# Performance work log

Measured on AMD Instinct MI355X. Metric: run time of the kernel, lower is better.

The kernel has to match this reference:

```python
import jax, jax.numpy as jnp
import numpy as np

STRIDE = (1, 1)
PAD = (1, 1)
DIL = (1, 1)
KH, KW = 3, 3
DEFORM_GROUPS = 2


def setup_inputs() -> dict:
    key = jax.random.key(0)
    ks = jax.random.split(key, 5)
    B, C, H, W = 4, 128, 64, 64
    Cout = 128
    K = KH * KW
    n = C * KH * KW
    stdv = 1.0 / np.sqrt(n)
    x = jax.random.normal(ks[0], (B, C, H, W), dtype=jnp.float32)
    offset = jax.random.normal(ks[1], (B, DEFORM_GROUPS * 2 * K, H, W), dtype=jnp.float32)
    mask = jax.random.uniform(ks[2], (B, DEFORM_GROUPS * K, H, W), dtype=jnp.float32)
    weight = jax.random.uniform(ks[3], (Cout, C, KH, KW), minval=-stdv, maxval=stdv, dtype=jnp.float32)
    bias = jnp.zeros((Cout,), dtype=jnp.float32)
    return {"x": x, "offset": offset, "mask": mask, "weight": weight, "bias": bias}


def _mdcn_forward(x, offset, mask, weight, bias):
    B, C, H, W = x.shape
    Cout, Cin_g, kh, kw = weight.shape
    K = kh * kw
    dg = offset.shape[1] // (2 * K)
    Cg = C // dg
    sh, sw = STRIDE
    ph, pw = PAD
    dh, dw = DIL
    Ho = (H + 2 * ph - (dh * (kh - 1) + 1)) // sh + 1
    Wo = (W + 2 * pw - (dw * (kw - 1) + 1)) // sw + 1

    # offsets: (B, dg, K, 2, Ho, Wo) with (dy, dx) pairs; mask: (B, dg, K, Ho, Wo)
    off = offset.reshape(B, dg, K, 2, Ho, Wo)
    m = mask.reshape(B, dg, K, Ho, Wo)

    ky, kx = jnp.meshgrid(jnp.arange(kh), jnp.arange(kw), indexing="ij")
    ky = ky.reshape(K).astype(x.dtype)  # kernel tap row offsets
    kx = kx.reshape(K).astype(x.dtype)
    oy = (jnp.arange(Ho) * sh - ph).astype(x.dtype)
    ox = (jnp.arange(Wo) * sw - pw).astype(x.dtype)

    # sampling positions (B, dg, K, Ho, Wo)
    py = off[:, :, :, 0] + oy[None, None, None, :, None] + (ky * dh)[None, None, :, None, None]
    px = off[:, :, :, 1] + ox[None, None, None, None, :] + (kx * dw)[None, None, :, None, None]

    y0 = jnp.floor(py)
    x0 = jnp.floor(px)
    ly = py - y0
    lx = px - x0
    y0i = y0.astype(jnp.int32)
    x0i = x0.astype(jnp.int32)

    xg = x.reshape(B, dg, Cg, H * W)

    def gather(yi, xi):
        valid = (yi >= 0) & (yi < H) & (xi >= 0) & (xi < W)
        idx = jnp.clip(yi, 0, H - 1) * W + jnp.clip(xi, 0, W - 1)  # (B,dg,K,Ho,Wo)
        g = jax.vmap(jax.vmap(lambda xf, ix: xf[:, ix]))(xg, idx.reshape(B, dg, K * Ho * Wo))
        g = g.reshape(B, dg, Cg, K, Ho, Wo)
        return g * valid[:, :, None].astype(x.dtype)

    w00 = ((1 - ly) * (1 - lx))[:, :, None]
    w01 = ((1 - ly) * lx)[:, :, None]
    w10 = (ly * (1 - lx))[:, :, None]
    w11 = (ly * lx)[:, :, None]

    val = (w00 * gather(y0i, x0i)
           + w01 * gather(y0i, x0i + 1)
           + w10 * gather(y0i + 1, x0i)
           + w11 * gather(y0i + 1, x0i + 1))

    # modulation and im2col-GEMM (groups=1): col (B, C*K, Ho*Wo)
    col = (val * m[:, :, None]).reshape(B, C * K, Ho * Wo)
    wk = weight.reshape(Cout, C * K)
    out = jnp.einsum("ok,bkp->bop", wk, col).reshape(B, Cout, Ho, Wo)
    return out + bias[None, :, None, None]


def reference(x, offset, mask, weight, bias):
    return _mdcn_forward(x, offset, mask, weight, bias)
```

## Files before the change

### kernel.cpp

```cpp
#include <hip/hip_runtime.h>
#include <hip/hip_fp16.h>

#define B_    4
#define C_    128
#define H_    64
#define W_    64
#define CO_   128
#define K_    9
#define DG_   2
#define HW_   4096
#define CK_   1152
#define NKT_  36
#define NPAIR_ 576
#define PSTR_ 68
#define PLSZ_ 4352

typedef __attribute__((ext_vector_type(8))) short  short8;
typedef __attribute__((ext_vector_type(4))) float  floatx4;
typedef float f2v __attribute__((ext_vector_type(2), aligned(4)));

__device__ __align__(16) unsigned short g_wA[NKT_ * 8 * 64 * 8];
__device__ __align__(16) unsigned int   g_colu[(size_t)B_ * 128 * NPAIR_ * 32];
__device__ __align__(16) int4           g_desc[B_ * DG_ * K_ * HW_];

__device__ __forceinline__ unsigned short f32_to_bf16(float f) {
    unsigned int u = __float_as_uint(f);
    u += 0x7FFFu + ((u >> 16) & 1u);
    return (unsigned short)(u >> 16);
}
__device__ __forceinline__ unsigned int pack_bf16x2(float a, float b) {
    return (unsigned int)f32_to_bf16(a) | ((unsigned int)f32_to_bf16(b) << 16);
}

__global__ __launch_bounds__(256) void prep_kernel(
    const float* __restrict__ w,
    const float* __restrict__ offset,
    const float* __restrict__ mask)
{
    const int bid = blockIdx.x;
    if (bid < 576) {
        const int lin  = bid * 256 + threadIdx.x;
        const int j    = lin & 7;
        const int lane = (lin >> 3) & 63;
        const int mtkt = lin >> 9;
        const int mt   = mtkt & 7;
        const int kt   = mtkt >> 3;
        const int co   = mt * 16 + (lane & 15);
        const int k    = kt * 32 + (lane >> 4) * 8 + j;
        g_wA[lin] = f32_to_bf16(w[co * CK_ + k]);
    } else {
        const int lin = (bid - 576) * 256 + threadIdx.x;
        const int pix = lin & (HW_ - 1);
        const int bgk = lin >> 12;
        const int k   = bgk % 9;
        const int bg  = bgk / 9;
        const int ho = pix >> 6;
        const int wo = pix & 63;
        const int ky = k / 3;
        const int kx = k - 3 * ky;

        const float py = offset[(size_t)(bg * 18 + 2 * k)     * HW_ + pix] + (float)(ho - 1 + ky);
        const float px = offset[(size_t)(bg * 18 + 2 * k + 1) * HW_ + pix] + (float)(wo - 1 + kx);
        const float m  = mask  [(size_t)(bg * 9 + k)          * HW_ + pix];

        const float y0f = floorf(py);
        const float x0f = floorf(px);
        const float ly = py - y0f;
        const float lx = px - x0f;
        const int y0 = (int)y0f;
        const int x0 = (int)x0f;

        const bool yin = (y0 >= 0) & (y0 <= H_ - 2);
        const float er0 = yin ? (1.0f - ly) : ((y0 == -1)     ? ly          : 0.0f);
        const float er1 = yin ? ly          : ((y0 == H_ - 1) ? (1.0f - ly) : 0.0f);
        const bool xin = (x0 >= 0) & (x0 <= W_ - 2);
        const float ec0 = xin ? (1.0f - lx) : ((x0 == -1)     ? lx          : 0.0f);
        const float ec1 = xin ? lx          : ((x0 == W_ - 1) ? (1.0f - lx) : 0.0f);
        const int yc = min(max(y0, 0), H_ - 2);
        const int xc = min(max(x0, 0), W_ - 2);

        const __half2 wlo = __floats2half2_rn(m * er0 * ec0, m * er0 * ec1);
        const __half2 whi = __floats2half2_rn(m * er1 * ec0, m * er1 * ec1);
        int4 d;
        d.x = yc * PSTR_ + xc;
        d.y = __builtin_bit_cast(int, wlo);
        d.z = __builtin_bit_cast(int, whi);
        d.w = 0;
        g_desc[lin] = d;
    }
}

__global__ __launch_bounds__(1024, 4) void col_kernel(const float* __restrict__ x)
{
    const int bid = blockIdx.x;
    const int b   = bid >> 6;
    const int cp  = bid & 63;
    const int c0  = cp * 2;
    const int g   = c0 >> 6;
    const int t   = threadIdx.x;

    __shared__ __align__(16) float s_x[2 * PLSZ_];

    {
        const int ci = t >> 9;
        const int q  = t & 511;
        const float* __restrict__ src = x + (size_t)(b * C_ + c0 + ci) * HW_ + q * 8;
        const float4 v0 = *(const float4*)src;
        const float4 v1 = *(const float4*)(src + 4);
        float* dst = s_x + ci * PLSZ_ + (q >> 3) * PSTR_ + (q & 7) * 8;
        *(float4*)dst = v0;
        *(float4*)(dst + 4) = v1;
    }
    __syncthreads();

    const int4* __restrict__ descb = g_desc + (size_t)((b * DG_ + g) * 9) * HW_;

#pragma unroll
    for (int ps = 0; ps < 4; ++ps) {
        const int pix = ps * 1024 + t;
        const int pt  = pix >> 5;
        const int pl  = pix & 31;
        int4 d[9];
#pragma unroll
        for (int k = 0; k < 9; ++k) d[k] = descb[(size_t)k * HW_ + pix];

        float v[18];
#pragma unroll
        for (int k = 0; k < 9; ++k) {
            const float2 wl = __half22float2(__builtin_bit_cast(__half2, d[k].y));
            const float2 wh = __half22float2(__builtin_bit_cast(__half2, d[k].z));
#pragma unroll
            for (int ci = 0; ci < 2; ++ci) {
                const float* p = s_x + ci * PLSZ_ + d[k].x;
                const f2v lo = *(const f2v*)p;
                const f2v hi = *(const f2v*)(p + PSTR_);
                v[ci * 9 + k] = wl.x * lo.x + wl.y * lo.y + wh.x * hi.x + wh.y * hi.y;
            }
        }
        unsigned int* __restrict__ outb =
            g_colu + ((size_t)(b * 128 + pt) * NPAIR_ + cp * 9) * 32 + pl;
#pragma unroll
        for (int j = 0; j < 9; ++j)
            outb[j * 32] = pack_bf16x2(v[2 * j], v[2 * j + 1]);
    }
}

__global__ __launch_bounds__(512) void gemm_kernel(
    const float* __restrict__ bias, float* __restrict__ out)
{
    const int bid  = blockIdx.x;
    const int b    = bid >> 7;
    const int pt   = bid & 127;
    const int t    = threadIdx.x;
    const int w    = t >> 6;
    const int cw   = w >> 1;
    const int nt   = w & 1;
    const int lane = t & 63;
    const int l15  = lane & 15;
    const int quad = lane >> 4;

    const unsigned short* __restrict__ ap = g_wA + ((size_t)(cw * 2) * 64 + lane) * 8;
    const unsigned int* __restrict__ bp =
        g_colu + ((size_t)(b * 128 + pt) * NPAIR_ + quad * 4) * 32 + nt * 16 + l15;

    floatx4 acc0 = {0.f, 0.f, 0.f, 0.f};
    floatx4 acc1 = {0.f, 0.f, 0.f, 0.f};

    short8 a0c = *(const short8*)ap;
    short8 a1c = *(const short8*)(ap + 512);
    uint4 u0;
    u0.x = bp[0]; u0.y = bp[32]; u0.z = bp[64]; u0.w = bp[96];
    short8 b_c = __builtin_bit_cast(short8, u0);

#pragma unroll 4
    for (int kt = 0; kt < NKT_; ++kt) {
        short8 a0n = a0c, a1n = a1c, b_n = b_c;
        if (kt < NKT_ - 1) {
            const unsigned short* an = ap + (size_t)(kt + 1) * 4096;
            a0n = *(const short8*)an;
            a1n = *(const short8*)(an + 512);
            const unsigned int* bq = bp + (size_t)(kt + 1) * 512;
            uint4 u;
            u.x = bq[0]; u.y = bq[32]; u.z = bq[64]; u.w = bq[96];
            b_n = __builtin_bit_cast(short8, u);
        }
        acc0 = __builtin_amdgcn_mfma_f32_16x16x32_bf16(a0c, b_c, acc0, 0, 0, 0);
        acc1 = __builtin_amdgcn_mfma_f32_16x16x32_bf16(a1c, b_c, acc1, 0, 0, 0);
        a0c = a0n; a1c = a1n; b_c = b_n;
    }

#pragma unroll
    for (int mtl = 0; mtl < 2; ++mtl) {
        const floatx4 a = mtl ? acc1 : acc0;
        const int cob = cw * 32 + mtl * 16 + quad * 4;
#pragma unroll
        for (int r = 0; r < 4; ++r) {
            const int co = cob + r;
            out[((size_t)(b * CO_ + co) << 12) + pt * 32 + nt * 16 + l15] = a[r] + bias[co];
        }
    }
}

extern "C" void kernel_launch(void* const* d_in, const int* in_sizes, int n_in,
                              void* d_out, int out_size, void* d_ws, size_t ws_size,
                              hipStream_t stream) {
    const float* x      = (const float*)d_in[0];
    const float* offset = (const float*)d_in[1];
    const float* mask   = (const float*)d_in[2];
    const float* weight = (const float*)d_in[3];
    const float* bias   = (const float*)d_in[4];
    float* out = (float*)d_out;

    hipLaunchKernelGGL(prep_kernel, dim3(576 + 1152), dim3(256), 0, stream, weight, offset, mask);
    hipLaunchKernelGGL(col_kernel, dim3(B_ * 64), dim3(1024), 0, stream, x);
    hipLaunchKernelGGL(gemm_kernel, dim3(B_ * 128), dim3(512), 0, stream, bias, out);
}
```

Measured before the change: 102.6 us.

## Stage four fp16 channels per shared texel and reorder GEMM K dimension tap-major

The col kernel now loads four channels into shared memory as packed fp16 vectors, so one bilinear descriptor fetch serves four channels and each corner read is a single 8-byte LDS load. The block split changes to 4-channel by quarter-image tiles with one pixel per thread. The reduction dimension is reordered tap-major, with weights permuted to match. The GEMM uses 64-pixel tiles with 16 waves per block. Storing x in fp16 adds some precision loss, and there are fewer, larger GEMM blocks.

```diff
diff --git a/kernel.cpp b/kernel.cpp
--- a/kernel.cpp
+++ b/kernel.cpp
@@ -12,15 +12,14 @@
 #define CK_   1152
 #define NKT_  36
 #define NPAIR_ 576
-#define PSTR_ 68
-#define PLSZ_ 4352
-
-typedef __attribute__((ext_vector_type(8))) short  short8;
-typedef __attribute__((ext_vector_type(4))) float  floatx4;
-typedef float f2v __attribute__((ext_vector_type(2), aligned(4)));
+#define XSTR_ 68
+
+typedef __attribute__((ext_vector_type(8))) short    short8;
+typedef __attribute__((ext_vector_type(4))) float    floatx4;
+typedef __attribute__((ext_vector_type(4))) _Float16 h4v;
 
 __device__ __align__(16) unsigned short g_wA[NKT_ * 8 * 64 * 8];
-__device__ __align__(16) unsigned int   g_colu[(size_t)B_ * 128 * NPAIR_ * 32];
+__device__ __align__(16) unsigned int   g_colu[(size_t)B_ * 64 * NPAIR_ * 64];
 __device__ __align__(16) int4           g_desc[B_ * DG_ * K_ * HW_];
 
 __device__ __forceinline__ unsigned short f32_to_bf16(float f) {
@@ -46,8 +45,10 @@
         const int mt   = mtkt & 7;
         const int kt   = mtkt >> 3;
         const int co   = mt * 16 + (lane & 15);
-        const int k    = kt * 32 + (lane >> 4) * 8 + j;
-        g_wA[lin] = f32_to_bf16(w[co * CK_ + k]);
+        const int kp   = kt * 32 + (lane >> 4) * 8 + j;
+        const int c    = kp & 127;
+        const int k    = kp >> 7;
+        g_wA[lin] = f32_to_bf16(w[co * CK_ + c * 9 + k]);
     } else {
         const int lin = (bid - 576) * 256 + threadIdx.x;
         const int pix = lin & (HW_ - 1);
@@ -82,7 +83,7 @@
         const __half2 wlo = __floats2half2_rn(m * er0 * ec0, m * er0 * ec1);
         const __half2 whi = __floats2half2_rn(m * er1 * ec0, m * er1 * ec1);
         int4 d;
-        d.x = yc * PSTR_ + xc;
+        d.x = yc * XSTR_ + xc;
         d.y = __builtin_bit_cast(int, wlo);
         d.z = __builtin_bit_cast(int, whi);
         d.w = 0;
@@ -90,78 +91,81 @@
     }
 }
 
-__global__ __launch_bounds__(1024, 4) void col_kernel(const float* __restrict__ x)
+__global__ __launch_bounds__(1024) void col_kernel(const float* __restrict__ x)
 {
     const int bid = blockIdx.x;
-    const int b   = bid >> 6;
-    const int cp  = bid & 63;
-    const int c0  = cp * 2;
-    const int g   = c0 >> 6;
+    const int b   = bid >> 7;
+    const int rem = bid & 127;
+    const int cq  = rem >> 2;
+    const int qu  = rem & 3;
+    const int c0  = cq * 4;
+    const int g   = cq >> 4;
     const int t   = threadIdx.x;
 
-    __shared__ __align__(16) float s_x[2 * PLSZ_];
+    __shared__ h4v s_x4[64 * XSTR_];
 
     {
-        const int ci = t >> 9;
-        const int q  = t & 511;
-        const float* __restrict__ src = x + (size_t)(b * C_ + c0 + ci) * HW_ + q * 8;
-        const float4 v0 = *(const float4*)src;
-        const float4 v1 = *(const float4*)(src + 4);
-        float* dst = s_x + ci * PLSZ_ + (q >> 3) * PSTR_ + (q & 7) * 8;
-        *(float4*)dst = v0;
-        *(float4*)(dst + 4) = v1;
+        const int p0  = t * 4;
+        const int row = p0 >> 6;
+        const int col = p0 & 63;
+        const float* __restrict__ src = x + ((size_t)(b * C_ + c0) << 12) + p0;
+        const float4 f0 = *(const float4*)(src);
+        const float4 f1 = *(const float4*)(src + HW_);
+        const float4 f2 = *(const float4*)(src + 2 * HW_);
+        const float4 f3 = *(const float4*)(src + 3 * HW_);
+        h4v* dst = s_x4 + row * XSTR_ + col;
+        dst[0] = h4v{(_Float16)f0.x, (_Float16)f1.x, (_Float16)f2.x, (_Float16)f3.x};
+        dst[1] = h4v{(_Float16)f0.y, (_Float16)f1.y, (_Float16)f2.y, (_Float16)f3.y};
+        dst[2] = h4v{(_Float16)f0.z, (_Float16)f1.z, (_Float16)f2.z, (_Float16)f3.z};
+        dst[3] = h4v{(_Float16)f0.w, (_Float16)f1.w, (_Float16)f2.w, (_Float16)f3.w};
     }
     __syncthreads();
 
-    const int4* __restrict__ descb = g_desc + (size_t)((b * DG_ + g) * 9) * HW_;
-
-#pragma unroll
-    for (int ps = 0; ps < 4; ++ps) {
-        const int pix = ps * 1024 + t;
-        const int pt  = pix >> 5;
-        const int pl  = pix & 31;
-        int4 d[9];
-#pragma unroll
-        for (int k = 0; k < 9; ++k) d[k] = descb[(size_t)k * HW_ + pix];
-
-        float v[18];
-#pragma unroll
-        for (int k = 0; k < 9; ++k) {
-            const float2 wl = __half22float2(__builtin_bit_cast(__half2, d[k].y));
-            const float2 wh = __half22float2(__builtin_bit_cast(__half2, d[k].z));
-#pragma unroll
-            for (int ci = 0; ci < 2; ++ci) {
-                const float* p = s_x + ci * PLSZ_ + d[k].x;
-                const f2v lo = *(const f2v*)p;
-                const f2v hi = *(const f2v*)(p + PSTR_);
-                v[ci * 9 + k] = wl.x * lo.x + wl.y * lo.y + wh.x * hi.x + wh.y * hi.y;
-            }
-        }
-        unsigned int* __restrict__ outb =
-            g_colu + ((size_t)(b * 128 + pt) * NPAIR_ + cp * 9) * 32 + pl;
-#pragma unroll
-        for (int j = 0; j < 9; ++j)
-            outb[j * 32] = pack_bf16x2(v[2 * j], v[2 * j + 1]);
-    }
-}
-
-__global__ __launch_bounds__(512) void gemm_kernel(
+    const int pix = qu * 1024 + t;
+    const int pt  = pix >> 6;
+    const int pl  = pix & 63;
+    const int4* __restrict__ descb =
+        g_desc + (size_t)((b * DG_ + g) * 9) * HW_ + pix;
+    unsigned int* __restrict__ outb =
+        g_colu + ((size_t)(b * 64 + pt) * NPAIR_ + 2 * cq) * 64 + pl;
+
+#pragma unroll
+    for (int k = 0; k < 9; ++k) {
+        const int4 d = descb[(size_t)k * HW_];
+        const float2 wl = __half22float2(__builtin_bit_cast(__half2, d.y));
+        const float2 wh = __half22float2(__builtin_bit_cast(__half2, d.z));
+        const h4v* p = s_x4 + d.x;
+        const h4v lo0 = p[0];
+        const h4v lo1 = p[1];
+        const h4v hi0 = p[XSTR_];
+        const h4v hi1 = p[XSTR_ + 1];
+        float v[4];
+#pragma unroll
+        for (int ci = 0; ci < 4; ++ci)
+            v[ci] = wl.x * (float)lo0[ci] + wl.y * (float)lo1[ci]
+                  + wh.x * (float)hi0[ci] + wh.y * (float)hi1[ci];
+        outb[k * 64 * 64]      = pack_bf16x2(v[0], v[1]);
+        outb[k * 64 * 64 + 64] = pack_bf16x2(v[2], v[3]);
+    }
+}
+
+__global__ __launch_bounds__(1024) void gemm_kernel(
     const float* __restrict__ bias, float* __restrict__ out)
 {
     const int bid  = blockIdx.x;
-    const int b    = bid >> 7;
-    const int pt   = bid & 127;
+    const int b    = bid >> 6;
+    const int pt   = bid & 63;
     const int t    = threadIdx.x;
     const int w    = t >> 6;
-    const int cw   = w >> 1;
-    const int nt   = w & 1;
+    const int cw   = w >> 2;
+    const int nt   = w & 3;
     const int lane = t & 63;
     const int l15  = lane & 15;
     const int quad = lane >> 4;
 
     const unsigned short* __restrict__ ap = g_wA + ((size_t)(cw * 2) * 64 + lane) * 8;
     const unsigned int* __restrict__ bp =
-        g_colu + ((size_t)(b * 128 + pt) * NPAIR_ + quad * 4) * 32 + nt * 16 + l15;
+        g_colu + ((size_t)(b * 64 + pt) * NPAIR_ + quad * 4) * 64 + nt * 16 + l15;
 
     floatx4 acc0 = {0.f, 0.f, 0.f, 0.f};
     floatx4 acc1 = {0.f, 0.f, 0.f, 0.f};
@@ -169,7 +173,7 @@
     short8 a0c = *(const short8*)ap;
     short8 a1c = *(const short8*)(ap + 512);
     uint4 u0;
-    u0.x = bp[0]; u0.y = bp[32]; u0.z = bp[64]; u0.w = bp[96];
+    u0.x = bp[0]; u0.y = bp[64]; u0.z = bp[128]; u0.w = bp[192];
     short8 b_c = __builtin_bit_cast(short8, u0);
 
 #pragma unroll 4
@@ -179,9 +183,9 @@
             const unsigned short* an = ap + (size_t)(kt + 1) * 4096;
             a0n = *(const short8*)an;
             a1n = *(const short8*)(an + 512);
-            const unsigned int* bq = bp + (size_t)(kt + 1) * 512;
+            const unsigned int* bq = bp + (size_t)(kt + 1) * 1024;
             uint4 u;
-            u.x = bq[0]; u.y = bq[32]; u.z = bq[64]; u.w = bq[96];
+            u.x = bq[0]; u.y = bq[64]; u.z = bq[128]; u.w = bq[192];
             b_n = __builtin_bit_cast(short8, u);
         }
         acc0 = __builtin_amdgcn_mfma_f32_16x16x32_bf16(a0c, b_c, acc0, 0, 0, 0);
@@ -189,6 +193,7 @@
         a0c = a0n; a1c = a1n; b_c = b_n;
     }
 
+    const int pixo = pt * 64 + nt * 16 + l15;
 #pragma unroll
     for (int mtl = 0; mtl < 2; ++mtl) {
         const floatx4 a = mtl ? acc1 : acc0;
@@ -196,7 +201,7 @@
 #pragma unroll
         for (int r = 0; r < 4; ++r) {
             const int co = cob + r;
-            out[((size_t)(b * CO_ + co) << 12) + pt * 32 + nt * 16 + l15] = a[r] + bias[co];
+            out[((size_t)(b * CO_ + co) << 12) + pixo] = a[r] + bias[co];
         }
     }
 }
@@ -212,6 +217,6 @@
     float* out = (float*)d_out;
 
     hipLaunchKernelGGL(prep_kernel, dim3(576 + 1152), dim3(256), 0, stream, weight, offset, mask);
-    hipLaunchKernelGGL(col_kernel, dim3(B_ * 64), dim3(1024), 0, stream, x);
-    hipLaunchKernelGGL(gemm_kernel, dim3(B_ * 128), dim3(512), 0, stream, bias, out);
-}
+    hipLaunchKernelGGL(col_kernel, dim3(512), dim3(1024), 0, stream, x);
+    hipLaunchKernelGGL(gemm_kernel, dim3(256), dim3(1024), 0, stream, bias, out);
+}
```

Result: faster. 100.3 us (-2.2%).
